# Kernel optimization log

Hardware: AMD Instinct MI355X
Metric: run time of the kernel (lower is better)

## Reference

```python
import jax, jax.numpy as jnp
import numpy as np

B, Q, K = 4, 1024, 2048
QDIM, MDIM, EDIM, H = 1024, 1024, 1024, 16
HD = EDIM // H

def setup_inputs() -> dict:
    key = jax.random.key(0)
    ks = jax.random.split(key, 7)
    s = lambda d: (1.0 / np.sqrt(d))
    return {
        'query': jax.random.normal(ks[0], (B, Q, QDIM), jnp.float32),
        'memory': jax.random.normal(ks[1], (B, K, MDIM), jnp.float32),
        'bias': jax.random.normal(ks[2], (B, K), jnp.float32),
        'Wq': jax.random.normal(ks[3], (QDIM, EDIM), jnp.float32) * s(QDIM),
        'Wk': jax.random.normal(ks[4], (MDIM, EDIM), jnp.float32) * s(MDIM),
        'Wv': jax.random.normal(ks[5], (MDIM, EDIM), jnp.float32) * s(MDIM),
        'Wo': jax.random.normal(ks[6], (EDIM, EDIM), jnp.float32) * s(EDIM),
    }

def reference(query, memory, bias, Wq, Wk, Wv, Wo):
    scale = HD ** -0.5
    # projections -> [B, H, Q/K, HD]
    q = (query @ Wq).reshape(B, Q, H, HD).transpose(0, 2, 1, 3)
    k = (memory @ Wk).reshape(B, K, H, HD).transpose(0, 2, 1, 3)
    v = (memory @ Wv).reshape(B, K, H, HD).transpose(0, 2, 1, 3)
    scores = jnp.einsum('bhqd,bhkd->bhqk', q, k) * scale
    scores = scores + bias[:, None, None, :]
    weights = jax.nn.softmax(scores, axis=-1)
    out = jnp.einsum('bhqk,bhkd->bhqd', weights, v)
    out = out.transpose(0, 2, 1, 3).reshape(B, Q, EDIM)
    return out @ Wo
```

## Files before the change

kernel.cpp:

```cpp
#include <hip/hip_runtime.h>
#include <cstdint>
#include <cstddef>

typedef unsigned short u16;
typedef __attribute__((ext_vector_type(8))) short bf16x8;
typedef __attribute__((ext_vector_type(4))) short bf16x4;
typedef __attribute__((ext_vector_type(4))) float f32x4;
typedef __attribute__((ext_vector_type(16))) float f32x16;

#define B_  4
#define Q_  1024
#define K_  2048
#define E_  1024
#define H_  16
#define HD_ 64
#define LOG2E 1.4426950408889634f
#define M0_  16.0f

__device__ inline u16 f2bf(float f) {
  union { float f; uint32_t u; } x; x.f = f;
  return (u16)((x.u + 0x7fffu + ((x.u >> 16) & 1u)) >> 16);
}

__device__ inline short bfc(float f) {
  __bf16 h = (__bf16)f;
  return __builtin_bit_cast(short, h);
}

__device__ inline void gload16(const u16* g, void* l) {
  __builtin_amdgcn_global_load_lds((const __attribute__((address_space(1))) void*)g,
                                   (__attribute__((address_space(3))) void*)l, 16, 0, 0);
}

#define NQ8 (B_ * Q_ * E_ / 8)
#define NM8 (B_ * K_ * E_ / 8)
#define NBI (B_ * K_)
#define NPREP ((NQ8 + NM8 + NBI) / 256)
__global__ __launch_bounds__(256) void prep_all(const float* __restrict__ query,
                                                const float* __restrict__ memory,
                                                const float* __restrict__ bias,
                                                const float* W0, const float* W1,
                                                const float* W2, const float* W3,
                                                u16* __restrict__ qb,
                                                u16* __restrict__ mb,
                                                float* __restrict__ bias2,
                                                u16* T0, u16* T1, u16* T2, u16* T3) {
  __shared__ float t[64][65];
  int bid = blockIdx.x;
  if (bid < NPREP) {
    int i = bid * 256 + threadIdx.x;
    const float* src;
    u16* dst;
    if (i < NQ8) {
      src = query + (size_t)i * 8; dst = qb + (size_t)i * 8;
    } else if (i < NQ8 + NM8) {
      int j = i - NQ8;
      src = memory + (size_t)j * 8; dst = mb + (size_t)j * 8;
    } else {
      int j = i - (NQ8 + NM8);
      if (j < NBI) bias2[j] = bias[j] * LOG2E - M0_;
      return;
    }
    float4 a = *reinterpret_cast<const float4*>(src);
    float4 b = *reinterpret_cast<const float4*>(src + 4);
    union { u16 u[8]; uint4 v; } r;
    r.u[0] = f2bf(a.x); r.u[1] = f2bf(a.y); r.u[2] = f2bf(a.z); r.u[3] = f2bf(a.w);
    r.u[4] = f2bf(b.x); r.u[5] = f2bf(b.y); r.u[6] = f2bf(b.z); r.u[7] = f2bf(b.w);
    *reinterpret_cast<uint4*>(dst) = r.v;
  } else {
    int tb = bid - NPREP;
    int z = tb >> 8, xy = tb & 255;
    const float* W; u16* T;
    switch (z) {
      case 0: W = W0; T = T0; break;
      case 1: W = W1; T = T1; break;
      case 2: W = W2; T = T2; break;
      default: W = W3; T = T3; break;
    }
    int k0 = (xy & 15) * 64, n0 = (xy >> 4) * 64;
    int r = threadIdx.x >> 6, c = threadIdx.x & 63;
#pragma unroll
    for (int i = 0; i < 16; ++i)
      t[r + i * 4][c] = W[(size_t)(k0 + r + i * 4) * E_ + n0 + c];
    __syncthreads();
#pragma unroll
    for (int i = 0; i < 16; ++i)
      T[(size_t)(n0 + r + i * 4) * E_ + k0 + c] = f2bf(t[c][r + i * 4]);
  }
}

template <int MODE>
__device__ __forceinline__ void gemm_body(const u16* __restrict__ A,
                                          const u16* __restrict__ Bt,
                                          void* __restrict__ C,
                                          int M, int N, int Kc, int bx, int by,
                                          char* lds) {
  const int tid = threadIdx.x;
  const int w = tid >> 6, l = tid & 63;
  const int wr = w >> 1, wc = w & 1;
  const int lr = l & 15, lg = l >> 4;
  const int m0 = bx * 128, n0 = by * 128;

  const int e0g = tid * 8, e1g = e0g + 2048;
  const int row0 = e0g >> 5, row1 = e1g >> 5;
  const int lc0 = ((((e0g & 31) >> 3) ^ ((row0 >> 1) & 3)) * 8);
  const int lc1 = ((((e1g & 31) >> 3) ^ ((row1 >> 1) & 3)) * 8);
  const u16* Ar0 = A  + (size_t)(m0 + row0) * Kc + lc0;
  const u16* Ar1 = A  + (size_t)(m0 + row1) * Kc + lc1;
  const u16* Br0 = Bt + (size_t)(n0 + row0) * Kc + lc0;
  const u16* Br1 = Bt + (size_t)(n0 + row1) * Kc + lc1;
  const int d0 = tid * 16, d1 = d0 + 4096;

  const int ck = (lg ^ ((lr >> 1) & 3)) * 16;
  int aofs = (wr * 64 + lr) * 64 + ck;
  int bofs = 16384 + (wc * 64 + lr) * 64 + ck;

  f32x4 acc[4][4];
#pragma unroll
  for (int mt = 0; mt < 4; ++mt)
#pragma unroll
    for (int nt = 0; nt < 4; ++nt)
      acc[mt][nt] = (f32x4){0.f, 0.f, 0.f, 0.f};

  gload16(Ar0, lds + d0);
  gload16(Ar1, lds + d1);
  gload16(Br0, lds + 16384 + d0);
  gload16(Br1, lds + 16384 + d1);
  __syncthreads();

  const int NI = Kc >> 5;
  for (int ki = 0; ki < NI; ++ki) {
    if (ki + 1 < NI) {
      const int nb = ((ki & 1) ^ 1) * 8192;
      const int kk = (ki + 1) * 32;
      gload16(Ar0 + kk, lds + nb + d0);
      gload16(Ar1 + kk, lds + nb + d1);
      gload16(Br0 + kk, lds + 16384 + nb + d0);
      gload16(Br1 + kk, lds + 16384 + nb + d1);
    }

    bf16x8 a[4], b[4];
#pragma unroll
    for (int mt = 0; mt < 4; ++mt)
      a[mt] = *reinterpret_cast<const bf16x8*>(lds + aofs + mt * 1024);
#pragma unroll
    for (int nt = 0; nt < 4; ++nt)
      b[nt] = *reinterpret_cast<const bf16x8*>(lds + bofs + nt * 1024);
    __builtin_amdgcn_s_setprio(1);
#pragma unroll
    for (int mt = 0; mt < 4; ++mt)
#pragma unroll
      for (int nt = 0; nt < 4; ++nt)
        acc[mt][nt] = __builtin_amdgcn_mfma_f32_16x16x32_bf16(a[mt], b[nt], acc[mt][nt], 0, 0, 0);
    __builtin_amdgcn_s_setprio(0);

    aofs ^= 8192; bofs ^= 8192;
    __syncthreads();
  }

#pragma unroll
  for (int mt = 0; mt < 4; ++mt) {
#pragma unroll
    for (int nt = 0; nt < 4; ++nt) {
      int col = n0 + wc * 64 + nt * 16 + lr;
#pragma unroll
      for (int j = 0; j < 4; ++j) {
        int row = m0 + wr * 64 + mt * 16 + lg * 4 + j;
        float v = acc[mt][nt][j];
        if (MODE == 0) {
          ((float*)C)[(size_t)row * N + col] = v;
        } else if (MODE == 1) {
          ((u16*)C)[(size_t)row * N + col] = f2bf(v);
        } else if (MODE == 3) {
          ((u16*)C)[(size_t)row * N + col] = f2bf(v * (0.125f * LOG2E));
        } else {
          ((u16*)C)[((size_t)((col >> 11) * 16 + (row >> 6)) * 64 + (row & 63)) * 2048 + (col & 2047)] = f2bf(v);
        }
      }
    }
  }
}

__global__ __launch_bounds__(256) void gemm_out(const u16* __restrict__ A,
                                                const u16* __restrict__ Bt,
                                                void* __restrict__ C,
                                                int M, int N, int Kc) {
  __shared__ uint4 lds4[2048];
  int d = blockIdx.x;
  int bid = (d & 7) * 32 + (d >> 3);
  gemm_body<0>(A, Bt, C, M, N, Kc, bid >> 3, bid & 7, (char*)lds4);
}

__global__ __launch_bounds__(256) void proj_fused(const u16* __restrict__ qb,
                                                  const u16* __restrict__ mb,
                                                  const u16* __restrict__ wqt,
                                                  const u16* __restrict__ wkt,
                                                  const u16* __restrict__ wvt,
                                                  u16* __restrict__ qproj,
                                                  u16* __restrict__ kproj,
                                                  u16* __restrict__ vt) {
  __shared__ uint4 lds4[2048];
  char* lds = (char*)lds4;
  int d = blockIdx.x;
  int bid = (d & 7) * 160 + (d >> 3);
  if (bid < 256) {
    gemm_body<3>(qb, wqt, qproj, B_ * Q_, E_, E_, bid >> 3, bid & 7, lds);
  } else if (bid < 768) {
    int i = bid - 256;
    gemm_body<1>(mb, wkt, kproj, B_ * K_, E_, E_, i >> 3, i & 7, lds);
  } else {
    int i = bid - 768;
    gemm_body<2>(wvt, mb, vt, E_, B_ * K_, E_, i & 7, i >> 3, lds);
  }
}

__global__ __launch_bounds__(256, 4) void attn_kernel(const u16* __restrict__ qp,
                                                      const u16* __restrict__ kp,
                                                      const u16* __restrict__ vT,
                                                      const float* __restrict__ bias2,
                                                      u16* __restrict__ out) {
  __shared__ uint4 lds4[2048];
  char* ldsb = (char*)lds4;

  const int blk = blockIdx.x;
  const int hg = blk & 63, qt = blk >> 6;
  const int b = hg >> 4, h = hg & 15;
  const int tid = threadIdx.x;
  const int w = tid >> 6, l = tid & 63;
  const int wq = w & 1, wk = w >> 1;
  const int l31 = l & 31, lh = l >> 5;

  const int bk4 = l31 >> 2;
  const int t4 = bk4 & 3;
  const int pk31 = (((t4 == 1) || (t4 == 2)) ? (bk4 ^ 3) : bk4) * 4 + (l31 & 3);

  bf16x8 qf[4];
  const u16* qrow = qp + (size_t)(b * Q_ + qt * 64 + wq * 32 + l31) * E_ + h * 64 + lh * 8;
#pragma unroll
  for (int st = 0; st < 4; ++st)
    qf[st] = *reinterpret_cast<const bf16x8*>(qrow + st * 16);

  f32x16 O0, O1;
#pragma unroll
  for (int i = 0; i < 16; ++i) { O0[i] = 0.f; O1[i] = 0.f; }
  float Osum = 0.f;

  const float* bias_b = bias2 + (size_t)b * K_;
  const u16* kbase = kp + (size_t)b * K_ * E_ + h * 64;
  const u16* vbase = vT + (size_t)(b * H_ + h) * HD_ * K_;

  const int xkk = (pk31 & 7) * 8;
  const int xvv = (l31 & 7) * 8;
  int kofs[4];
#pragma unroll
  for (int st = 0; st < 4; ++st)
    kofs[st] = (wk * 32 + pk31) * 128 + (((st * 16 + lh * 8) ^ xkk) << 1);
  int vofs[2];
#pragma unroll
  for (int ksl = 0; ksl < 2; ++ksl)
    vofs[ksl] = 16384 + l31 * 128 + (((wk * 32 + ksl * 16 + lh * 8) ^ xvv) << 1);
  const float* bbase = bias_b + wk * 32 + lh * 8;

  const int e0 = tid * 8, e1 = e0 + 2048;
  const int r0 = e0 >> 6, r1 = e1 >> 6;
  const int sc0 = (e0 & 63) ^ ((r0 & 7) * 8);
  const int sc1 = (e1 & 63) ^ ((r1 & 7) * 8);

  gload16(kbase + (size_t)r0 * E_ + sc0, ldsb + tid * 16);
  gload16(kbase + (size_t)r1 * E_ + sc1, ldsb + 4096 + tid * 16);
  gload16(vbase + (size_t)r0 * K_ + sc0, ldsb + 16384 + tid * 16);
  gload16(vbase + (size_t)r1 * K_ + sc1, ldsb + 16384 + 4096 + tid * 16);
  __syncthreads();

  const int NT = K_ / 64;
  for (int t = 0; t < NT; ++t) {
    if (t + 1 < NT) {
      const int nb = ((t & 1) ^ 1) * 8192;
      int kk0 = (t + 1) * 64;
      gload16(kbase + (size_t)(kk0 + r0) * E_ + sc0, ldsb + nb + tid * 16);
      gload16(kbase + (size_t)(kk0 + r1) * E_ + sc1, ldsb + nb + 4096 + tid * 16);
      gload16(vbase + (size_t)r0 * K_ + kk0 + sc0, ldsb + 16384 + nb + tid * 16);
      gload16(vbase + (size_t)r1 * K_ + kk0 + sc1, ldsb + 16384 + nb + 4096 + tid * 16);
    }

    const float* bt = bbase + t * 64;
    float4 bg0 = *reinterpret_cast<const float4*>(bt);
    float4 bg1 = *reinterpret_cast<const float4*>(bt + 4);
    float4 bg2 = *reinterpret_cast<const float4*>(bt + 16);
    float4 bg3 = *reinterpret_cast<const float4*>(bt + 20);
    f32x16 S;
    S[0] = bg0.x; S[1] = bg0.y; S[2] = bg0.z; S[3] = bg0.w;
    S[4] = bg1.x; S[5] = bg1.y; S[6] = bg1.z; S[7] = bg1.w;
    S[8] = bg2.x; S[9] = bg2.y; S[10] = bg2.z; S[11] = bg2.w;
    S[12] = bg3.x; S[13] = bg3.y; S[14] = bg3.z; S[15] = bg3.w;
    __builtin_amdgcn_s_setprio(1);
#pragma unroll
    for (int st = 0; st < 4; ++st) {
      bf16x8 ka = *reinterpret_cast<const bf16x8*>(ldsb + kofs[st]);
      S = __builtin_amdgcn_mfma_f32_32x32x16_bf16(ka, qf[st], S, 0, 0, 0);
    }
    __builtin_amdgcn_s_setprio(0);

#pragma unroll
    for (int i = 0; i < 16; ++i) S[i] = exp2f(S[i]);
    float ps = ((S[0] + S[1]) + (S[2] + S[3])) + ((S[4] + S[5]) + (S[6] + S[7]))
             + ((S[8] + S[9]) + (S[10] + S[11])) + ((S[12] + S[13]) + (S[14] + S[15]));
    ps += __shfl_xor(ps, 32, 64);
    Osum += ps;

    uint32_t u[8];
#pragma unroll
    for (int j = 0; j < 8; ++j) {
      float plo = S[2 * j], phi = S[2 * j + 1];
      asm("v_cvt_pk_bf16_f32 %0, %1, %2" : "=v"(u[j]) : "v"(plo), "v"(phi));
    }
    bf16x8 P0 = __builtin_bit_cast(bf16x8, (uint4){u[0], u[1], u[2], u[3]});
    bf16x8 P1 = __builtin_bit_cast(bf16x8, (uint4){u[4], u[5], u[6], u[7]});

    __builtin_amdgcn_s_setprio(1);
    {
      bf16x8 va;
      va = *reinterpret_cast<const bf16x8*>(ldsb + vofs[0]);
      O0 = __builtin_amdgcn_mfma_f32_32x32x16_bf16(va, P0, O0, 0, 0, 0);
      va = *reinterpret_cast<const bf16x8*>(ldsb + vofs[0] + 4096);
      O1 = __builtin_amdgcn_mfma_f32_32x32x16_bf16(va, P0, O1, 0, 0, 0);
      va = *reinterpret_cast<const bf16x8*>(ldsb + vofs[1]);
      O0 = __builtin_amdgcn_mfma_f32_32x32x16_bf16(va, P1, O0, 0, 0, 0);
      va = *reinterpret_cast<const bf16x8*>(ldsb + vofs[1] + 4096);
      O1 = __builtin_amdgcn_mfma_f32_32x32x16_bf16(va, P1, O1, 0, 0, 0);
    }
    __builtin_amdgcn_s_setprio(0);

    kofs[0] ^= 8192; kofs[1] ^= 8192; kofs[2] ^= 8192; kofs[3] ^= 8192;
    vofs[0] ^= 8192; vofs[1] ^= 8192;
    __syncthreads();
  }

  float* ex = (float*)ldsb + (size_t)(wq * 64 + l) * 33;
  if (wk == 1) {
#pragma unroll
    for (int i = 0; i < 16; ++i) ex[i] = O0[i];
#pragma unroll
    for (int i = 0; i < 16; ++i) ex[16 + i] = O1[i];
    ex[32] = Osum;
  }
  __syncthreads();
  if (wk == 0) {
#pragma unroll
    for (int i = 0; i < 16; ++i) O0[i] += ex[i];
#pragma unroll
    for (int i = 0; i < 16; ++i) O1[i] += ex[16 + i];
    Osum += ex[32];
    float inv = 1.f / Osum;
    u16* orow = out + (size_t)(b * Q_ + qt * 64 + wq * 32 + l31) * E_ + h * 64;
#pragma unroll
    for (int g = 0; g < 4; ++g) {
      int hd0 = 8 * g + 4 * lh;
#pragma unroll
      for (int j = 0; j < 4; ++j) {
        orow[hd0 + j] = (u16)bfc(O0[4 * g + j] * inv);
        orow[32 + hd0 + j] = (u16)bfc(O1[4 * g + j] * inv);
      }
    }
  }
}

extern "C" void kernel_launch(void* const* d_in, const int* in_sizes, int n_in,
                              void* d_out, int out_size, void* d_ws, size_t ws_size,
                              hipStream_t stream) {
  const float* query  = (const float*)d_in[0];
  const float* memory = (const float*)d_in[1];
  const float* bias   = (const float*)d_in[2];
  const float* Wq     = (const float*)d_in[3];
  const float* Wk     = (const float*)d_in[4];
  const float* Wv     = (const float*)d_in[5];
  const float* Wo     = (const float*)d_in[6];
  float* out = (float*)d_out;

  char* p = (char*)d_ws;
  u16* qb    = (u16*)p; p += (size_t)B_ * Q_ * E_ * 2;
  u16* mb    = (u16*)p; p += (size_t)B_ * K_ * E_ * 2;
  u16* wqt   = (u16*)p; p += (size_t)E_ * E_ * 2;
  u16* wkt   = (u16*)p; p += (size_t)E_ * E_ * 2;
  u16* wvt   = (u16*)p; p += (size_t)E_ * E_ * 2;
  u16* wot   = (u16*)p; p += (size_t)E_ * E_ * 2;
  u16* qproj = (u16*)p; p += (size_t)B_ * Q_ * E_ * 2;
  u16* kproj = (u16*)p; p += (size_t)B_ * K_ * E_ * 2;
  u16* vt    = (u16*)p; p += (size_t)B_ * K_ * E_ * 2;
  u16* attn  = (u16*)p; p += (size_t)B_ * Q_ * E_ * 2;
  float* bias2 = (float*)p; p += (size_t)B_ * K_ * 4;

  prep_all<<<NPREP + 1024, 256, 0, stream>>>(query, memory, bias, Wq, Wk, Wv, Wo,
                                             qb, mb, bias2, wqt, wkt, wvt, wot);

  proj_fused<<<1280, 256, 0, stream>>>(qb, mb, wqt, wkt, wvt, qproj, kproj, vt);

  attn_kernel<<<B_ * H_ * (Q_ / 64), 256, 0, stream>>>(qproj, kproj, vt, bias2, attn);

  gemm_out<<<256, 256, 0, stream>>>(attn, wot, out, B_ * Q_, E_, E_);
}
```

Baseline: 148.7 us.

## Widen output GEMM to 512 threads and prefetch bias in attention loop

The output projection GEMM gets its own kernel body with 8 waves per block. Each wave computes a 64x32 sub-tile instead of 64x64, which raises wave-level parallelism for the 256-block launch. In the attention kernel, the bias values for the next tile are loaded one iteration ahead. The cross-half row-sum shuffle moves out of the loop and runs once after it. Pointer increments replace recomputed addresses. The cost is more synchronisation participants per block and less work per wave in the GEMM.

```diff
diff --git a/kernel.cpp b/kernel.cpp
--- a/kernel.cpp
+++ b/kernel.cpp
@@ -167,9 +167,7 @@
       for (int j = 0; j < 4; ++j) {
         int row = m0 + wr * 64 + mt * 16 + lg * 4 + j;
         float v = acc[mt][nt][j];
-        if (MODE == 0) {
-          ((float*)C)[(size_t)row * N + col] = v;
-        } else if (MODE == 1) {
+        if (MODE == 1) {
           ((u16*)C)[(size_t)row * N + col] = f2bf(v);
         } else if (MODE == 3) {
           ((u16*)C)[(size_t)row * N + col] = f2bf(v * (0.125f * LOG2E));
@@ -181,14 +179,83 @@
   }
 }
 
-__global__ __launch_bounds__(256) void gemm_out(const u16* __restrict__ A,
+__global__ __launch_bounds__(512) void gemm_out(const u16* __restrict__ A,
                                                 const u16* __restrict__ Bt,
-                                                void* __restrict__ C,
-                                                int M, int N, int Kc) {
+                                                float* __restrict__ C,
+                                                int N, int Kc) {
   __shared__ uint4 lds4[2048];
+  char* lds = (char*)lds4;
   int d = blockIdx.x;
   int bid = (d & 7) * 32 + (d >> 3);
-  gemm_body<0>(A, Bt, C, M, N, Kc, bid >> 3, bid & 7, (char*)lds4);
+  const int bx = bid >> 3, by = bid & 7;
+  const int tid = threadIdx.x;
+  const int w = tid >> 6, l = tid & 63;
+  const int wrow = w >> 2, wcol = w & 3;
+  const int lr = l & 15, lg = l >> 4;
+  const int m0 = bx * 128, n0 = by * 128;
+
+  const int e = tid * 8;
+  const int row = e >> 5;
+  const int lc = ((((e & 31) >> 3) ^ ((row >> 1) & 3)) * 8);
+  const u16* Ar = A  + (size_t)(m0 + row) * Kc + lc;
+  const u16* Br = Bt + (size_t)(n0 + row) * Kc + lc;
+  const int dd = tid * 16;
+
+  const int ck = (lg ^ ((lr >> 1) & 3)) * 16;
+  int aofs = (wrow * 64 + lr) * 64 + ck;
+  int bofs = 16384 + (wcol * 32 + lr) * 64 + ck;
+
+  f32x4 acc[4][2];
+#pragma unroll
+  for (int mt = 0; mt < 4; ++mt)
+#pragma unroll
+    for (int nt = 0; nt < 2; ++nt)
+      acc[mt][nt] = (f32x4){0.f, 0.f, 0.f, 0.f};
+
+  gload16(Ar, lds + dd);
+  gload16(Br, lds + 16384 + dd);
+  __syncthreads();
+
+  const int NI = Kc >> 5;
+  for (int ki = 0; ki < NI; ++ki) {
+    if (ki + 1 < NI) {
+      const int nb = ((ki & 1) ^ 1) * 8192;
+      const int kk = (ki + 1) * 32;
+      gload16(Ar + kk, lds + nb + dd);
+      gload16(Br + kk, lds + 16384 + nb + dd);
+    }
+
+    bf16x8 a[4], b[2];
+#pragma unroll
+    for (int mt = 0; mt < 4; ++mt)
+      a[mt] = *reinterpret_cast<const bf16x8*>(lds + aofs + mt * 1024);
+#pragma unroll
+    for (int nt = 0; nt < 2; ++nt)
+      b[nt] = *reinterpret_cast<const bf16x8*>(lds + bofs + nt * 1024);
+    __builtin_amdgcn_s_setprio(1);
+#pragma unroll
+    for (int mt = 0; mt < 4; ++mt)
+#pragma unroll
+      for (int nt = 0; nt < 2; ++nt)
+        acc[mt][nt] = __builtin_amdgcn_mfma_f32_16x16x32_bf16(a[mt], b[nt], acc[mt][nt], 0, 0, 0);
+    __builtin_amdgcn_s_setprio(0);
+
+    aofs ^= 8192; bofs ^= 8192;
+    __syncthreads();
+  }
+
+#pragma unroll
+  for (int mt = 0; mt < 4; ++mt) {
+#pragma unroll
+    for (int nt = 0; nt < 2; ++nt) {
+      int col = n0 + wcol * 32 + nt * 16 + lr;
+#pragma unroll
+      for (int j = 0; j < 4; ++j) {
+        int rowc = m0 + wrow * 64 + mt * 16 + lg * 4 + j;
+        C[(size_t)rowc * N + col] = acc[mt][nt][j];
+      }
+    }
+  }
 }
 
 __global__ __launch_bounds__(256) void proj_fused(const u16* __restrict__ qb,
@@ -243,7 +310,7 @@
   f32x16 O0, O1;
 #pragma unroll
   for (int i = 0; i < 16; ++i) { O0[i] = 0.f; O1[i] = 0.f; }
-  float Osum = 0.f;
+  float OsumL = 0.f;
 
   const float* bias_b = bias2 + (size_t)b * K_;
   const u16* kbase = kp + (size_t)b * K_ * E_ + h * 64;
@@ -259,40 +326,55 @@
 #pragma unroll
   for (int ksl = 0; ksl < 2; ++ksl)
     vofs[ksl] = 16384 + l31 * 128 + (((wk * 32 + ksl * 16 + lh * 8) ^ xvv) << 1);
-  const float* bbase = bias_b + wk * 32 + lh * 8;
+
+  const float* btp = bias_b + wk * 32 + lh * 8;
+  float4 bg0 = *reinterpret_cast<const float4*>(btp);
+  float4 bg1 = *reinterpret_cast<const float4*>(btp + 4);
+  float4 bg2 = *reinterpret_cast<const float4*>(btp + 16);
+  float4 bg3 = *reinterpret_cast<const float4*>(btp + 20);
 
   const int e0 = tid * 8, e1 = e0 + 2048;
   const int r0 = e0 >> 6, r1 = e1 >> 6;
   const int sc0 = (e0 & 63) ^ ((r0 & 7) * 8);
   const int sc1 = (e1 & 63) ^ ((r1 & 7) * 8);
-
-  gload16(kbase + (size_t)r0 * E_ + sc0, ldsb + tid * 16);
-  gload16(kbase + (size_t)r1 * E_ + sc1, ldsb + 4096 + tid * 16);
-  gload16(vbase + (size_t)r0 * K_ + sc0, ldsb + 16384 + tid * 16);
-  gload16(vbase + (size_t)r1 * K_ + sc1, ldsb + 16384 + 4096 + tid * 16);
+  const u16* kp0 = kbase + (size_t)r0 * E_ + sc0;
+  const u16* kp1 = kbase + (size_t)r1 * E_ + sc1;
+  const u16* vp0 = vbase + (size_t)r0 * K_ + sc0;
+  const u16* vp1 = vbase + (size_t)r1 * K_ + sc1;
+
+  gload16(kp0, ldsb + tid * 16);
+  gload16(kp1, ldsb + 4096 + tid * 16);
+  gload16(vp0, ldsb + 16384 + tid * 16);
+  gload16(vp1, ldsb + 16384 + 4096 + tid * 16);
   __syncthreads();
 
   const int NT = K_ / 64;
   for (int t = 0; t < NT; ++t) {
     if (t + 1 < NT) {
       const int nb = ((t & 1) ^ 1) * 8192;
-      int kk0 = (t + 1) * 64;
-      gload16(kbase + (size_t)(kk0 + r0) * E_ + sc0, ldsb + nb + tid * 16);
-      gload16(kbase + (size_t)(kk0 + r1) * E_ + sc1, ldsb + nb + 4096 + tid * 16);
-      gload16(vbase + (size_t)r0 * K_ + kk0 + sc0, ldsb + 16384 + nb + tid * 16);
-      gload16(vbase + (size_t)r1 * K_ + kk0 + sc1, ldsb + 16384 + nb + 4096 + tid * 16);
-    }
-
-    const float* bt = bbase + t * 64;
-    float4 bg0 = *reinterpret_cast<const float4*>(bt);
-    float4 bg1 = *reinterpret_cast<const float4*>(bt + 4);
-    float4 bg2 = *reinterpret_cast<const float4*>(bt + 16);
-    float4 bg3 = *reinterpret_cast<const float4*>(bt + 20);
+      kp0 += (size_t)64 * E_; kp1 += (size_t)64 * E_;
+      vp0 += 64; vp1 += 64;
+      gload16(kp0, ldsb + nb + tid * 16);
+      gload16(kp1, ldsb + nb + 4096 + tid * 16);
+      gload16(vp0, ldsb + 16384 + nb + tid * 16);
+      gload16(vp1, ldsb + 16384 + nb + 4096 + tid * 16);
+    }
+
     f32x16 S;
     S[0] = bg0.x; S[1] = bg0.y; S[2] = bg0.z; S[3] = bg0.w;
     S[4] = bg1.x; S[5] = bg1.y; S[6] = bg1.z; S[7] = bg1.w;
     S[8] = bg2.x; S[9] = bg2.y; S[10] = bg2.z; S[11] = bg2.w;
     S[12] = bg3.x; S[13] = bg3.y; S[14] = bg3.z; S[15] = bg3.w;
+
+    float4 ng0 = bg0, ng1 = bg1, ng2 = bg2, ng3 = bg3;
+    if (t + 1 < NT) {
+      btp += 64;
+      ng0 = *reinterpret_cast<const float4*>(btp);
+      ng1 = *reinterpret_cast<const float4*>(btp + 4);
+      ng2 = *reinterpret_cast<const float4*>(btp + 16);
+      ng3 = *reinterpret_cast<const float4*>(btp + 20);
+    }
+
     __builtin_amdgcn_s_setprio(1);
 #pragma unroll
     for (int st = 0; st < 4; ++st) {
@@ -305,8 +387,7 @@
     for (int i = 0; i < 16; ++i) S[i] = exp2f(S[i]);
     float ps = ((S[0] + S[1]) + (S[2] + S[3])) + ((S[4] + S[5]) + (S[6] + S[7]))
              + ((S[8] + S[9]) + (S[10] + S[11])) + ((S[12] + S[13]) + (S[14] + S[15]));
-    ps += __shfl_xor(ps, 32, 64);
-    Osum += ps;
+    OsumL += ps;
 
     uint32_t u[8];
 #pragma unroll
@@ -331,10 +412,13 @@
     }
     __builtin_amdgcn_s_setprio(0);
 
+    bg0 = ng0; bg1 = ng1; bg2 = ng2; bg3 = ng3;
     kofs[0] ^= 8192; kofs[1] ^= 8192; kofs[2] ^= 8192; kofs[3] ^= 8192;
     vofs[0] ^= 8192; vofs[1] ^= 8192;
     __syncthreads();
   }
+
+  float Osum = OsumL + __shfl_xor(OsumL, 32, 64);
 
   float* ex = (float*)ldsb + (size_t)(wq * 64 + l) * 33;
   if (wk == 1) {
@@ -397,5 +481,5 @@
 
   attn_kernel<<<B_ * H_ * (Q_ / 64), 256, 0, stream>>>(qproj, kproj, vt, bias2, attn);
 
-  gemm_out<<<256, 256, 0, stream>>>(attn, wot, out, B_ * Q_, E_, E_);
-}
+  gemm_out<<<256, 512, 0, stream>>>(attn, wot, out, E_, E_);
+}
```

After: 146.0 us. About the same (-1.8%).
